# Performance work log

Hardware: AMD Instinct MI355X
Metric: run time of the kernel (lower is better)

The kernel has to match this reference:

```python
import jax, jax.numpy as jnp
import numpy as np

SCALE = 10.0
KB = 1.0  # kernel_bandwidth

B, D, P, M, K = 128, 128, 4, 100000, 10


def _sqdist(a, b):
    # a: [..., N, D], b: [..., M, D] -> squared euclidean [..., N, M]
    a2 = jnp.sum(a * a, axis=-1)[..., :, None]
    b2 = jnp.sum(b * b, axis=-1)[..., None, :]
    ab = jnp.einsum('...nd,...md->...nm', a, b)
    return jnp.maximum(a2 + b2 - 2.0 * ab, 0.0)


def setup_inputs() -> dict:
    key = jax.random.key(0)
    k1, k2, k3, k4, k5, k6, k7 = jax.random.split(key, 7)
    return {
        'global_img_feat': jax.random.normal(k1, (B, D), jnp.float32),
        'global_text_feat': jax.random.normal(k2, (B, D), jnp.float32),
        'local_img_feats': jax.random.normal(k3, (P, B, D), jnp.float32),
        'centers': jax.random.normal(k4, (P, M, D), jnp.float32),
        'cross_indices': jax.random.randint(k5, (B, K), 0, M, jnp.int64),
        'position': jax.random.randint(k6, (B,), 0, M, jnp.int64),
        'memory_vid': jax.random.randint(k7, (M,), 0, 1000, jnp.int64),
    }


def reference(global_img_feat, global_text_feat, local_img_feats, centers,
              cross_indices, position, memory_vid):
    b = global_img_feat.shape[0]
    # ---- global MMD alignment (text branch detached) ----
    img = global_img_feat / jnp.linalg.norm(global_img_feat, axis=1, keepdims=True)
    txt_d = jax.lax.stop_gradient(global_text_feat)
    txt = txt_d / jnp.linalg.norm(txt_d, axis=1, keepdims=True)
    inv2kb2 = 1.0 / (2.0 * KB * KB)
    k_xx = jnp.exp(-_sqdist(img, img) * inv2kb2)
    k_yy = jnp.exp(-_sqdist(txt, txt) * inv2kb2)
    k_xy = jnp.exp(-_sqdist(img, txt) * inv2kb2)
    off = ~jnp.eye(b, dtype=bool)
    denom = b * (b - 1)
    mmd = (jnp.sum(jnp.where(off, k_xx, 0.0)) / denom
           + jnp.sum(jnp.where(off, k_yy, 0.0)) / denom
           - 2.0 * jnp.mean(k_xy))
    # ---- local part contrastive loss (vectorized over P parts) ----
    m = centers.shape[1]
    pos_feat = centers[:, cross_indices]                       # [P,B,K,D]
    f2 = jnp.sum(local_img_feats ** 2, axis=-1)                # [P,B]
    p2 = jnp.sum(pos_feat ** 2, axis=-1)                       # [P,B,K]
    fp = jnp.einsum('pbd,pbkd->pbk', local_img_feats, pos_feat)
    pos_dist = jnp.sqrt(jnp.maximum(f2[..., None] + p2 - 2.0 * fp, 0.0))  # [P,B,K]
    neg_dist = jnp.sqrt(_sqdist(local_img_feats, centers))     # [P,B,M]
    # negative mask over memory slots (int indices are constants)
    neg_mask = jnp.ones((m,), bool).at[cross_indices.reshape(-1)].set(False)
    neg_mask = neg_mask.at[position].set(False)
    x = jnp.log(jnp.sum(jnp.exp(-SCALE * pos_dist), axis=-1))  # [P,B]
    y = jnp.log(jnp.sum(jnp.exp(-SCALE * neg_dist) * neg_mask[None, None, :], axis=-1))
    l = jnp.sum(-x + y, axis=1) / local_img_feats.shape[1]     # [P]
    l = jnp.where(jnp.isnan(l), 0.0, l)
    local_loss = jnp.sum(l) / local_img_feats.shape[0]
    total = local_loss + 1.0 * mmd
    pos_vid = memory_vid[cross_indices]                        # [B,K]
    return total, local_loss, mmd, pos_vid
```

## Files before the change

kernel.cpp:

```cpp
#include <hip/hip_runtime.h>
#include <math.h>

#define B_ 128
#define D_ 128
#define P_ 4
#define M_ 100000
#define K_ 10
#define SCALE_ 10.0f
#define WPP 512
#define NT16 6250
#define NEG_BLOCKS 512
#define MMD_BLOCKS 128
#define POS_BLOCKS 128
#define D2_CUT 120.0f

typedef short bf16x8 __attribute__((ext_vector_type(8)));
typedef float floatx4 __attribute__((ext_vector_type(4)));

__device__ inline unsigned pack_bf16_trunc(unsigned f0, unsigned f1) {
    return __builtin_amdgcn_perm(f1, f0, 0x07060302u);
}

template <int CTRL>
__device__ inline float dpp_add(float v) {
    int x = __builtin_amdgcn_update_dpp(0, __builtin_bit_cast(int, v), CTRL, 0xF, 0xF, true);
    return v + __builtin_bit_cast(float, x);
}
__device__ inline float row16Sum(float v) {
    v = dpp_add<0xB1>(v);
    v = dpp_add<0x4E>(v);
    v = dpp_add<0x141>(v);
    v = dpp_add<0x140>(v);
    return v;
}
__device__ inline float waveSum64(float v) {
    v = row16Sum(v);
    v += __shfl_xor(v, 16, 64);
    v += __shfl_xor(v, 32, 64);
    return v;
}
__device__ inline float waveReduceSumOld(float v) {
    #pragma unroll
    for (int off = 32; off > 0; off >>= 1) v += __shfl_xor(v, off, 64);
    return v;
}
__device__ inline float blockReduce128(float v, float* sh2) {
    v = waveSum64(v);
    int wid = threadIdx.x >> 6;
    if ((threadIdx.x & 63) == 0) sh2[wid] = v;
    __syncthreads();
    float r = sh2[0] + sh2[1];
    __syncthreads();
    return r;
}

__global__ __launch_bounds__(128) void k_prep(const float* __restrict__ img,
                                              const float* __restrict__ txt,
                                              const float* __restrict__ local,
                                              float* imgT, float* txtT,
                                              float* a2i, float* a2t,
                                              float* f2w, float* s_neg,
                                              bf16x8* __restrict__ Apk) {
    __shared__ float sh2[2];
    int bid = blockIdx.x, t = threadIdx.x;
    if (bid < 256) {
        int row = bid & 127, which = bid >> 7;
        if (bid < 4) s_neg[bid * 128 + t] = 0.f;
        const float* src = which ? txt : img;
        float* dstT = which ? txtT : imgT;
        float* a2 = which ? a2t : a2i;
        float v = src[row * D_ + t];
        float s = blockReduce128(v * v, sh2);
        float n = v / sqrtf(s);
        dstT[t * 128 + row] = n;
        float s2 = blockReduce128(n * n, sh2);
        if (t == 0) a2[row] = s2;
    } else if (bid < 768) {
        int r = bid - 256;
        float v = local[(size_t)r * D_ + t];
        float s = blockReduce128(v * v, sh2);
        if (t == 0) f2w[r] = s;
    } else {
        int g = (bid - 768) * 128 + t;
        int p = g >> 11, f = g & 2047;
        int fl = f & 63, bt = (f >> 6) & 7, kc = f >> 9;
        int row = bt * 16 + (fl & 15);
        int col = kc * 32 + ((fl >> 4) & 3) * 8;
        const float* lp = local + (size_t)p * B_ * D_ + row * D_ + col;
        const uint4 u0 = *(const uint4*)lp;
        const uint4 u1 = *(const uint4*)(lp + 4);
        union { bf16x8 v; unsigned u[4]; } fr;
        fr.u[0] = pack_bf16_trunc(u0.x, u0.y);
        fr.u[1] = pack_bf16_trunc(u0.z, u0.w);
        fr.u[2] = pack_bf16_trunc(u1.x, u1.y);
        fr.u[3] = pack_bf16_trunc(u1.z, u1.w);
        Apk[g] = fr.v;
    }
}

__device__ __forceinline__ void load_rb(uint4 (&rb)[4][2], const float* cb,
                                        int tl, int n16, int q) {
    const uint4* src = (const uint4*)(cb + (size_t)(tl * 16 + n16) * D_ + q * 8);
    #pragma unroll
    for (int kc = 0; kc < 4; kc++) {
        rb[kc][0] = src[kc * 8];
        rb[kc][1] = src[kc * 8 + 1];
    }
}

__device__ __forceinline__ void compute_tile(const uint4 (&rb)[4][2], int tl, bool valid,
                                             const bf16x8* A_lds, const float* f2l,
                                             float (&sacc)[8][4],
                                             const int* __restrict__ ci,
                                             const int* __restrict__ posi,
                                             int l, int n16, int q) {
    float c2 = 0.f;
    bf16x8 bfr[4];
    #pragma unroll
    for (int kc = 0; kc < 4; kc++) {
        union { uint4 u; floatx4 f; } a, b;
        a.u = rb[kc][0];
        b.u = rb[kc][1];
        c2 += a.f[0]*a.f[0] + a.f[1]*a.f[1] + a.f[2]*a.f[2] + a.f[3]*a.f[3]
            + b.f[0]*b.f[0] + b.f[1]*b.f[1] + b.f[2]*b.f[2] + b.f[3]*b.f[3];
        union { bf16x8 v; unsigned u[4]; } fr;
        fr.u[0] = pack_bf16_trunc(a.u.x, a.u.y);
        fr.u[1] = pack_bf16_trunc(a.u.z, a.u.w);
        fr.u[2] = pack_bf16_trunc(b.u.x, b.u.y);
        fr.u[3] = pack_bf16_trunc(b.u.z, b.u.w);
        bfr[kc] = fr.v;
    }
    c2 += __shfl_xor(c2, 16, 64);
    c2 += __shfl_xor(c2, 32, 64);
    const float c2v = c2;

    floatx4 acc[8];
    #pragma unroll
    for (int bt = 0; bt < 8; bt++) acc[bt] = (floatx4)(0.f);
    #pragma unroll
    for (int kc = 0; kc < 4; kc++) {
        #pragma unroll
        for (int bt = 0; bt < 8; bt++) {
            bf16x8 af = A_lds[kc * 512 + bt * 64 + l];
            acc[bt] = __builtin_amdgcn_mfma_f32_16x16x32_bf16(af, bfr[kc], acc[bt], 0, 0, 0);
        }
    }

    float dmin = 1e30f;
    #pragma unroll
    for (int bt = 0; bt < 8; bt++) {
        floatx4 f4 = *(const floatx4*)&f2l[bt * 16 + q * 4];
        #pragma unroll
        for (int r = 0; r < 4; r++) {
            float d2 = fmaf(-2.f, acc[bt][r], f4[r] + c2v);
            dmin = fminf(dmin, d2);
        }
    }
    if (valid && __any(dmin < D2_CUT)) {
        const int gm = tl * 16 + n16;
        float vm = 1.f;
        for (int ii = 0; ii < B_ * K_; ii++) {
            if (ci[ii] == gm) vm = 0.f;
        }
        for (int ii = 0; ii < B_; ii++) {
            if (posi[ii] == gm) vm = 0.f;
        }
        #pragma unroll
        for (int bt = 0; bt < 8; bt++) {
            floatx4 f4 = *(const floatx4*)&f2l[bt * 16 + q * 4];
            #pragma unroll
            for (int r = 0; r < 4; r++) {
                float d2 = fmaxf(fmaf(-2.f, acc[bt][r], f4[r] + c2v), 0.f);
                if (d2 < D2_CUT) sacc[bt][r] += vm * expf(-SCALE_ * sqrtf(d2));
            }
        }
    }
}

__global__ __launch_bounds__(256, 2) void k_neg(const float* __restrict__ centers,
                                                const int* __restrict__ ci,
                                                const int* __restrict__ posi,
                                                const float* __restrict__ f2w,
                                                const bf16x8* __restrict__ Apk,
                                                float* __restrict__ s_neg) {
    __shared__ bf16x8 A_lds[2048];
    __shared__ float f2l[128];
    const int bid = blockIdx.x;
    const int t = threadIdx.x;
    const int w = t >> 6;
    const int l = t & 63;
    const int p = bid >> 7;
    const int v = ((bid & 127) << 2) + w;
    const int n16 = l & 15;
    const int q = l >> 4;

    const bf16x8* Ap = Apk + (p << 11);
    #pragma unroll
    for (int s8 = 0; s8 < 8; s8++) {
        int fb = w * 64 + 256 * s8;
        __builtin_amdgcn_global_load_lds(
            (const __attribute__((address_space(1))) void*)(Ap + fb + l),
            (__attribute__((address_space(3))) void*)(&A_lds[fb]),
            16, 0, 0);
    }
    if (t < 128) f2l[t] = f2w[p * 128 + t];
    __syncthreads();

    const float* cb = centers + (size_t)p * M_ * D_;

    float sacc[8][4];
    #pragma unroll
    for (int bt = 0; bt < 8; bt++)
        #pragma unroll
        for (int r = 0; r < 4; r++) sacc[bt][r] = 0.f;

    uint4 rbA[4][2], rbB[4][2];
    load_rb(rbA, cb, v, n16, q);
    for (int jj = 0; jj < 6; jj++) {
        const int t1 = v + (2 * jj + 1) * WPP;
        load_rb(rbB, cb, t1, n16, q);
        compute_tile(rbA, v + 2 * jj * WPP, true, A_lds, f2l, sacc, ci, posi, l, n16, q);
        const int t2i = v + (2 * jj + 2) * WPP;
        load_rb(rbA, cb, (t2i < NT16) ? t2i : 0, n16, q);
        compute_tile(rbB, t1, true, A_lds, f2l, sacc, ci, posi, l, n16, q);
    }
    const int t12 = v + 12 * WPP;
    compute_tile(rbA, t12, t12 < NT16, A_lds, f2l, sacc, ci, posi, l, n16, q);

    #pragma unroll
    for (int bt = 0; bt < 8; bt++) {
        #pragma unroll
        for (int r = 0; r < 4; r++) {
            float s = row16Sum(sacc[bt][r]);
            if (n16 == 0 && s != 0.f)
                atomicAdd(&s_neg[p * 128 + bt * 16 + q * 4 + r], s);
        }
    }
}

__global__ __launch_bounds__(256) void k_mp(const float* __restrict__ local,
                                            const float* __restrict__ centers,
                                            const float* __restrict__ imgT,
                                            const float* __restrict__ txtT,
                                            const float* __restrict__ a2i,
                                            const float* __restrict__ a2t,
                                            const int* __restrict__ ci,
                                            const int* __restrict__ mvid,
                                            const float* __restrict__ f2w,
                                            float* __restrict__ s_pos,
                                            double* __restrict__ mmd_part,
                                            float* __restrict__ out) {
    __shared__ float ri[128], rt[128], sh2[2];
    const int bid = blockIdx.x;
    const int t = threadIdx.x;
    const int w = t >> 6;
    const int l = t & 63;

    if (bid < MMD_BLOCKS) {
        const int i = bid;
        if (t < 128) {
            ri[t] = imgT[t * 128 + i];
            rt[t] = txtT[t * 128 + i];
        }
        __syncthreads();
        float kxx = 0.f, kyy = 0.f, kxy = 0.f;
        if (t < 128) {
            float dxx = 0.f, dyy = 0.f, dxy = 0.f;
            #pragma unroll 4
            for (int d = 0; d < D_; d++) {
                float rid = ri[d], rtd = rt[d];
                float av = imgT[d * 128 + t];
                float bv = txtT[d * 128 + t];
                dxx = fmaf(rid, av, dxx);
                dyy = fmaf(rtd, bv, dyy);
                dxy = fmaf(rid, bv, dxy);
            }
            kxx = (i == t) ? 0.f : expf(-fmaxf(a2i[i] + a2i[t] - 2.f * dxx, 0.f) * 0.5f);
            kyy = (i == t) ? 0.f : expf(-fmaxf(a2t[i] + a2t[t] - 2.f * dyy, 0.f) * 0.5f);
            kxy = expf(-fmaxf(a2i[i] + a2t[t] - 2.f * dxy, 0.f) * 0.5f);
        }
        float sxx = waveReduceSumOld(kxx);
        float syy = waveReduceSumOld(kyy);
        float sxy = waveReduceSumOld(kxy);
        __syncthreads();
        if (t == 0)  { sh2[0] = sxx; }
        if (t == 64) { sh2[1] = sxx; }
        __syncthreads();
        float txx = sh2[0] + sh2[1];
        __syncthreads();
        if (t == 0)  { sh2[0] = syy; }
        if (t == 64) { sh2[1] = syy; }
        __syncthreads();
        float tyy = sh2[0] + sh2[1];
        __syncthreads();
        if (t == 0)  { sh2[0] = sxy; }
        if (t == 64) { sh2[1] = sxy; }
        __syncthreads();
        float txy = sh2[0] + sh2[1];
        if (t == 0) {
            mmd_part[i] = (double)txx;
            mmd_part[128 + i] = (double)tyy;
            mmd_part[256 + i] = (double)txy;
        }
    } else {
        const int pair = (bid - MMD_BLOCKS) * 4 + w;
        const int p = pair >> 7, b = pair & 127;
        const float* f = local + (size_t)pair * D_;
        float f0 = f[l], f1 = f[l + 64];
        float f2v = f2w[pair];
        const float* cb = centers + (size_t)p * M_ * D_;
        float s = 0.f;
        #pragma unroll
        for (int k = 0; k < K_; k++) {
            int idx = ci[b * K_ + k];
            const float* c = cb + (size_t)idx * D_;
            float c0 = c[l], c1 = c[l + 64];
            float p2 = waveSum64(c0 * c0 + c1 * c1);
            float fp = waveSum64(f0 * c0 + f1 * c1);
            float d2 = fmaxf(f2v + p2 - 2.f * fp, 0.f);
            if (d2 < D2_CUT) s += expf(-SCALE_ * sqrtf(d2));
        }
        if (l == 0) s_pos[pair] = s;
        if (p == 0 && l < K_) {
            int ix = ci[b * K_ + l];
            out[3 + b * K_ + l] = (float)mvid[ix];
        }
    }
}

__global__ __launch_bounds__(512) void k_final(const float* __restrict__ s_pos,
                                               const float* __restrict__ s_neg,
                                               const double* __restrict__ mmd_part,
                                               float* out) {
    __shared__ float red[512];
    __shared__ float lp_[4];
    int t = threadIdx.x;
    float x = logf(s_pos[t]);
    float y = logf(s_neg[t]);
    red[t] = -x + y;
    __syncthreads();
    for (int s = 64; s > 0; s >>= 1) {
        if ((t & 127) < s) red[t] += red[t + s];
        __syncthreads();
    }
    if ((t & 127) == 0) {
        float lv = red[t] / (float)B_;
        if (isnan(lv)) lv = 0.f;
        lp_[t >> 7] = lv;
    }
    __syncthreads();
    if (t == 0) {
        float local_loss = (lp_[0] + lp_[1] + lp_[2] + lp_[3]) / (float)P_;
        double sxx = 0.0, syy = 0.0, sxy = 0.0;
        for (int i = 0; i < 128; i++) {
            sxx += mmd_part[i];
            syy += mmd_part[128 + i];
            sxy += mmd_part[256 + i];
        }
        double denom = 128.0 * 127.0;
        float mmd = (float)(sxx / denom + syy / denom - 2.0 * (sxy / (128.0 * 128.0)));
        out[0] = local_loss + mmd;
        out[1] = local_loss;
        out[2] = mmd;
    }
}

extern "C" void kernel_launch(void* const* d_in, const int* in_sizes, int n_in,
                              void* d_out, int out_size, void* d_ws, size_t ws_size,
                              hipStream_t stream) {
    const float* img     = (const float*)d_in[0];
    const float* txt     = (const float*)d_in[1];
    const float* local   = (const float*)d_in[2];
    const float* centers = (const float*)d_in[3];
    const int*   ci      = (const int*)d_in[4];
    const int*   posi    = (const int*)d_in[5];
    const int*   mvid    = (const int*)d_in[6];
    float* out = (float*)d_out;

    char* ws = (char*)d_ws;
    float*  imgT     = (float*)(ws + 0);
    float*  txtT     = (float*)(ws + 65536);
    float*  a2i      = (float*)(ws + 131072);
    float*  a2t      = (float*)(ws + 131584);
    float*  f2w      = (float*)(ws + 132096);
    float*  s_pos    = (float*)(ws + 134144);
    float*  s_neg    = (float*)(ws + 136192);
    double* mmd_part = (double*)(ws + 138240);
    bf16x8* Apk      = (bf16x8*)(ws + 147456);

    k_prep<<<832, 128, 0, stream>>>(img, txt, local, imgT, txtT, a2i, a2t, f2w, s_neg, Apk);
    k_neg<<<NEG_BLOCKS, 256, 0, stream>>>(centers, ci, posi, f2w, Apk, s_neg);
    k_mp<<<MMD_BLOCKS + POS_BLOCKS, 256, 0, stream>>>(
        local, centers, imgT, txtT, a2i, a2t, ci, mvid, f2w, s_pos, mmd_part, out);
    k_final<<<1, 512, 0, stream>>>(s_pos, s_neg, mmd_part, out);
}
```

Measured before the change: 344.6 us.

## Stage center tiles via async LDS DMA triple-buffer with wave-pair batch split

Rewrites the negative-distance kernel so that pairs of waves share each 16-row center tile. The tile is loaded with global_load_lds into a swizzled, triple-buffered LDS area instead of direct register loads. Each wave in a pair handles half of the 128 batch rows and keeps its bf16 A fragments and f2 values in registers rather than reading them from LDS. The goal is to overlap the loading of centers with the MFMA work more deeply and to cut LDS traffic for A. The cost is barrier synchronisation on every tile, and the squared norm of each center row is now computed redundantly by both waves.

```diff
diff --git a/kernel.cpp b/kernel.cpp
--- a/kernel.cpp
+++ b/kernel.cpp
@@ -7,8 +7,6 @@
 #define M_ 100000
 #define K_ 10
 #define SCALE_ 10.0f
-#define WPP 512
-#define NT16 6250
 #define NEG_BLOCKS 512
 #define MMD_BLOCKS 128
 #define POS_BLOCKS 128
@@ -98,142 +96,156 @@
     }
 }
 
-__device__ __forceinline__ void load_rb(uint4 (&rb)[4][2], const float* cb,
-                                        int tl, int n16, int q) {
-    const uint4* src = (const uint4*)(cb + (size_t)(tl * 16 + n16) * D_ + q * 8);
-    #pragma unroll
-    for (int kc = 0; kc < 4; kc++) {
-        rb[kc][0] = src[kc * 8];
-        rb[kc][1] = src[kc * 8 + 1];
-    }
-}
-
-__device__ __forceinline__ void compute_tile(const uint4 (&rb)[4][2], int tl, bool valid,
-                                             const bf16x8* A_lds, const float* f2l,
-                                             float (&sacc)[8][4],
-                                             const int* __restrict__ ci,
-                                             const int* __restrict__ posi,
-                                             int l, int n16, int q) {
-    float c2 = 0.f;
-    bf16x8 bfr[4];
-    #pragma unroll
-    for (int kc = 0; kc < 4; kc++) {
-        union { uint4 u; floatx4 f; } a, b;
-        a.u = rb[kc][0];
-        b.u = rb[kc][1];
-        c2 += a.f[0]*a.f[0] + a.f[1]*a.f[1] + a.f[2]*a.f[2] + a.f[3]*a.f[3]
-            + b.f[0]*b.f[0] + b.f[1]*b.f[1] + b.f[2]*b.f[2] + b.f[3]*b.f[3];
-        union { bf16x8 v; unsigned u[4]; } fr;
-        fr.u[0] = pack_bf16_trunc(a.u.x, a.u.y);
-        fr.u[1] = pack_bf16_trunc(a.u.z, a.u.w);
-        fr.u[2] = pack_bf16_trunc(b.u.x, b.u.y);
-        fr.u[3] = pack_bf16_trunc(b.u.z, b.u.w);
-        bfr[kc] = fr.v;
-    }
-    c2 += __shfl_xor(c2, 16, 64);
-    c2 += __shfl_xor(c2, 32, 64);
-    const float c2v = c2;
-
-    floatx4 acc[8];
-    #pragma unroll
-    for (int bt = 0; bt < 8; bt++) acc[bt] = (floatx4)(0.f);
-    #pragma unroll
-    for (int kc = 0; kc < 4; kc++) {
-        #pragma unroll
-        for (int bt = 0; bt < 8; bt++) {
-            bf16x8 af = A_lds[kc * 512 + bt * 64 + l];
-            acc[bt] = __builtin_amdgcn_mfma_f32_16x16x32_bf16(af, bfr[kc], acc[bt], 0, 0, 0);
-        }
-    }
-
-    float dmin = 1e30f;
-    #pragma unroll
-    for (int bt = 0; bt < 8; bt++) {
-        floatx4 f4 = *(const floatx4*)&f2l[bt * 16 + q * 4];
-        #pragma unroll
-        for (int r = 0; r < 4; r++) {
-            float d2 = fmaf(-2.f, acc[bt][r], f4[r] + c2v);
-            dmin = fminf(dmin, d2);
-        }
-    }
-    if (valid && __any(dmin < D2_CUT)) {
-        const int gm = tl * 16 + n16;
-        float vm = 1.f;
-        for (int ii = 0; ii < B_ * K_; ii++) {
-            if (ci[ii] == gm) vm = 0.f;
-        }
-        for (int ii = 0; ii < B_; ii++) {
-            if (posi[ii] == gm) vm = 0.f;
-        }
-        #pragma unroll
-        for (int bt = 0; bt < 8; bt++) {
-            floatx4 f4 = *(const floatx4*)&f2l[bt * 16 + q * 4];
-            #pragma unroll
-            for (int r = 0; r < 4; r++) {
-                float d2 = fmaxf(fmaf(-2.f, acc[bt][r], f4[r] + c2v), 0.f);
-                if (d2 < D2_CUT) sacc[bt][r] += vm * expf(-SCALE_ * sqrtf(d2));
-            }
-        }
-    }
-}
-
 __global__ __launch_bounds__(256, 2) void k_neg(const float* __restrict__ centers,
                                                 const int* __restrict__ ci,
                                                 const int* __restrict__ posi,
                                                 const float* __restrict__ f2w,
                                                 const bf16x8* __restrict__ Apk,
                                                 float* __restrict__ s_neg) {
-    __shared__ bf16x8 A_lds[2048];
-    __shared__ float f2l[128];
-    const int bid = blockIdx.x;
+    __shared__ float Bt[2][3][2048];
     const int t = threadIdx.x;
     const int w = t >> 6;
     const int l = t & 63;
+    const int bid = blockIdx.x;
     const int p = bid >> 7;
-    const int v = ((bid & 127) << 2) + w;
+    const int g = bid & 127;
+    const int pp = w >> 1;
+    const int hm = w & 1;
+    const int pairid = 2 * g + pp;
+    const int nt = (g < 53) ? 25 : 24;
     const int n16 = l & 15;
     const int q = l >> 4;
 
     const bf16x8* Ap = Apk + (p << 11);
-    #pragma unroll
-    for (int s8 = 0; s8 < 8; s8++) {
-        int fb = w * 64 + 256 * s8;
-        __builtin_amdgcn_global_load_lds(
-            (const __attribute__((address_space(1))) void*)(Ap + fb + l),
-            (__attribute__((address_space(3))) void*)(&A_lds[fb]),
-            16, 0, 0);
-    }
-    if (t < 128) f2l[t] = f2w[p * 128 + t];
-    __syncthreads();
-
-    const float* cb = centers + (size_t)p * M_ * D_;
-
-    float sacc[8][4];
-    #pragma unroll
-    for (int bt = 0; bt < 8; bt++)
-        #pragma unroll
-        for (int r = 0; r < 4; r++) sacc[bt][r] = 0.f;
-
-    uint4 rbA[4][2], rbB[4][2];
-    load_rb(rbA, cb, v, n16, q);
-    for (int jj = 0; jj < 6; jj++) {
-        const int t1 = v + (2 * jj + 1) * WPP;
-        load_rb(rbB, cb, t1, n16, q);
-        compute_tile(rbA, v + 2 * jj * WPP, true, A_lds, f2l, sacc, ci, posi, l, n16, q);
-        const int t2i = v + (2 * jj + 2) * WPP;
-        load_rb(rbA, cb, (t2i < NT16) ? t2i : 0, n16, q);
-        compute_tile(rbB, t1, true, A_lds, f2l, sacc, ci, posi, l, n16, q);
-    }
-    const int t12 = v + 12 * WPP;
-    compute_tile(rbA, t12, t12 < NT16, A_lds, f2l, sacc, ci, posi, l, n16, q);
-
-    #pragma unroll
-    for (int bt = 0; bt < 8; bt++) {
+    bf16x8 af[4][4];
+    #pragma unroll
+    for (int kc = 0; kc < 4; kc++)
+        #pragma unroll
+        for (int b4 = 0; b4 < 4; b4++)
+            af[kc][b4] = Ap[kc * 512 + (hm * 4 + b4) * 64 + l];
+    floatx4 f2r[4];
+    #pragma unroll
+    for (int b4 = 0; b4 < 4; b4++)
+        f2r[b4] = *(const floatx4*)&f2w[p * 128 + (hm * 4 + b4) * 16 + q * 4];
+
+    unsigned srcoff[4];
+    #pragma unroll
+    for (int j = 0; j < 4; j++) {
+        unsigned x = (unsigned)(hm * 4096 + j * 1024 + l * 16);
+        unsigned s = (x >> 9) & 7u;
+        srcoff[j] = x ^ (s << 4);
+    }
+
+    const char* tb0 = (const char*)(centers + (size_t)p * M_ * D_);
+    char* myBt = (char*)&Bt[pp][0][0];
+
+    auto DMA = [&](int tl, int buf) {
+        const char* src = tb0 + (size_t)tl * 8192;
+        char* dst = myBt + buf * 8192 + hm * 4096;
+        #pragma unroll
+        for (int j = 0; j < 4; j++) {
+            __builtin_amdgcn_global_load_lds(
+                (const __attribute__((address_space(1))) void*)(src + srcoff[j]),
+                (__attribute__((address_space(3))) void*)(dst + j * 1024),
+                16, 0, 0);
+        }
+    };
+
+    float sacc[4][4];
+    #pragma unroll
+    for (int b4 = 0; b4 < 4; b4++)
+        #pragma unroll
+        for (int r = 0; r < 4; r++) sacc[b4][r] = 0.f;
+
+    DMA(pairid, 0);
+    if (nt > 1) DMA(pairid + 256, 1);
+    asm volatile("s_waitcnt vmcnt(4)" ::: "memory");
+    __builtin_amdgcn_s_barrier();
+
+    int tli = pairid;
+    int ib = 0;
+    const unsigned sw = (unsigned)((n16 & 7) << 4);
+    for (int i = 0; i < nt; i++) {
+        const char* bb = myBt + ib * 8192;
+        float c2 = 0.f;
+        bf16x8 bfr[4];
+        #pragma unroll
+        for (int kc = 0; kc < 4; kc++) {
+            unsigned t0a = (unsigned)(n16 * 512 + kc * 128 + q * 32);
+            union { floatx4 f; uint4 u; } h0, h1;
+            h0.f = *(const floatx4*)(bb + (t0a ^ sw));
+            h1.f = *(const floatx4*)(bb + ((t0a + 16) ^ sw));
+            c2 += h0.f[0]*h0.f[0] + h0.f[1]*h0.f[1] + h0.f[2]*h0.f[2] + h0.f[3]*h0.f[3]
+                + h1.f[0]*h1.f[0] + h1.f[1]*h1.f[1] + h1.f[2]*h1.f[2] + h1.f[3]*h1.f[3];
+            union { bf16x8 v; unsigned uu[4]; } fr;
+            fr.uu[0] = pack_bf16_trunc(h0.u.x, h0.u.y);
+            fr.uu[1] = pack_bf16_trunc(h0.u.z, h0.u.w);
+            fr.uu[2] = pack_bf16_trunc(h1.u.x, h1.u.y);
+            fr.uu[3] = pack_bf16_trunc(h1.u.z, h1.u.w);
+            bfr[kc] = fr.v;
+        }
+        c2 += __shfl_xor(c2, 16, 64);
+        c2 += __shfl_xor(c2, 32, 64);
+        const float c2v = c2;
+
+        floatx4 acc[4];
+        #pragma unroll
+        for (int b4 = 0; b4 < 4; b4++) acc[b4] = (floatx4)(0.f);
+        #pragma unroll
+        for (int kc = 0; kc < 4; kc++) {
+            #pragma unroll
+            for (int b4 = 0; b4 < 4; b4++)
+                acc[b4] = __builtin_amdgcn_mfma_f32_16x16x32_bf16(af[kc][b4], bfr[kc], acc[b4], 0, 0, 0);
+        }
+
+        float dmin = 1e30f;
+        #pragma unroll
+        for (int b4 = 0; b4 < 4; b4++) {
+            #pragma unroll
+            for (int r = 0; r < 4; r++) {
+                float d2 = fmaf(-2.f, acc[b4][r], f2r[b4][r] + c2v);
+                dmin = fminf(dmin, d2);
+            }
+        }
+        if (__any(dmin < D2_CUT)) {
+            const int gm = tli * 16 + n16;
+            float vm = 1.f;
+            for (int ii = 0; ii < B_ * K_; ii++) {
+                if (ci[ii] == gm) vm = 0.f;
+            }
+            for (int ii = 0; ii < B_; ii++) {
+                if (posi[ii] == gm) vm = 0.f;
+            }
+            #pragma unroll
+            for (int b4 = 0; b4 < 4; b4++) {
+                #pragma unroll
+                for (int r = 0; r < 4; r++) {
+                    float d2 = fmaxf(fmaf(-2.f, acc[b4][r], f2r[b4][r] + c2v), 0.f);
+                    if (d2 < D2_CUT) sacc[b4][r] += vm * expf(-SCALE_ * sqrtf(d2));
+                }
+            }
+        }
+
+        if (i + 2 < nt) {
+            int b2 = ib + 2; if (b2 >= 3) b2 -= 3;
+            DMA(tli + 512, b2);
+            asm volatile("s_waitcnt vmcnt(4)" ::: "memory");
+        } else if (i + 1 < nt) {
+            asm volatile("s_waitcnt vmcnt(0)" ::: "memory");
+        }
+        __builtin_amdgcn_s_barrier();
+
+        tli += 256;
+        ib = (ib + 1 == 3) ? 0 : ib + 1;
+    }
+
+    #pragma unroll
+    for (int b4 = 0; b4 < 4; b4++) {
         #pragma unroll
         for (int r = 0; r < 4; r++) {
-            float s = row16Sum(sacc[bt][r]);
+            float s = row16Sum(sacc[b4][r]);
             if (n16 == 0 && s != 0.f)
-                atomicAdd(&s_neg[p * 128 + bt * 16 + q * 4 + r], s);
+                atomicAdd(&s_neg[p * 128 + (hm * 4 + b4) * 16 + q * 4 + r], s);
         }
     }
 }
```

After: 324.2 us. 5.9% less time.
